# Kernel tuning notes

Measured on AMD Instinct MI355X. Metric: run time of the kernel, lower is better.

Reference implementation:

```python
import jax, jax.numpy as jnp
import numpy as np

N_NODES = 100000
N_EDGES = 1600000
IN_FEATS = 512
OUT_FEATS = 128


def setup_inputs() -> dict:
    key = jax.random.key(0)
    k1, k2, k3, k4, k5 = jax.random.split(key, 5)
    feat = jax.random.normal(k1, (N_NODES, IN_FEATS), dtype=jnp.float32)
    src = jax.random.randint(k2, (N_EDGES,), 0, N_NODES, dtype=jnp.int32)
    dst = jax.random.randint(k3, (N_EDGES,), 0, N_NODES, dtype=jnp.int32)
    edge_weight = jax.random.uniform(k4, (N_EDGES,), dtype=jnp.float32)
    # xavier_uniform init for the [in, out] weight
    limit = float(np.sqrt(6.0 / (IN_FEATS + OUT_FEATS)))
    weight = jax.random.uniform(k5, (IN_FEATS, OUT_FEATS), dtype=jnp.float32,
                                minval=-limit, maxval=limit)
    bias = jnp.zeros((OUT_FEATS,), dtype=jnp.float32)
    return {"feat": feat, "weight": weight, "bias": bias,
            "edge_weight": edge_weight, "src": src, "dst": dst}


def reference(feat, weight, bias, edge_weight, src, dst):
    n = feat.shape[0]
    ones = jnp.ones_like(edge_weight)
    # degrees from edge list; clamp(min=1)
    out_deg = jnp.maximum(jax.ops.segment_sum(ones, src, num_segments=n), 1.0)
    in_deg = jnp.maximum(jax.ops.segment_sum(ones, dst, num_segments=n), 1.0)
    # norm='both': left-normalize source feats by out_deg^-0.5
    feat_src = feat * jax.lax.rsqrt(out_deg)[:, None]
    # in_feats > out_feats -> project before aggregation
    h = feat_src @ weight                      # [N, OUT]
    msg = h[src] * edge_weight[:, None]        # u_mul_e, [E, OUT]
    rst = jax.ops.segment_sum(msg, dst, num_segments=n)  # fn.sum per dst
    # right-normalize by in_deg^-0.5, add bias (activation is None)
    rst = rst * jax.lax.rsqrt(in_deg)[:, None] + bias
    return rst
```

## Files before the change

### kernel.cpp

```cpp
#include <hip/hip_runtime.h>
#include <hip/hip_bf16.h>

#define NNODES 100000
#define NEDGES 1600000
#define INF 512
#define OUTF 128
#define NB 391
#define BCAP 5120
#define SEG 4096

typedef __attribute__((ext_vector_type(8))) __bf16 bf16x8;
typedef __attribute__((ext_vector_type(4))) float f32x4;
typedef __attribute__((ext_vector_type(2))) float f32x2;

__global__ void wt_kernel(const float* __restrict__ w, unsigned short* __restrict__ wt) {
  int i = blockIdx.x * blockDim.x + threadIdx.x;
  if (i < OUTF * INF) {
    int n = i >> 9;
    int k = i & 511;
    __bf16 b = (__bf16)(w[k * OUTF + n]);
    wt[i] = __builtin_bit_cast(unsigned short, b);
  }
}

__global__ __launch_bounds__(256) void bucket_kernel(
    const int* __restrict__ src, const int* __restrict__ dst,
    const float* __restrict__ ew, int* __restrict__ out_cnt,
    int* __restrict__ bucket_cnt, int2* __restrict__ bucket) {
  __shared__ int hist[NB];
  __shared__ int base[NB];
  int t = threadIdx.x;
  for (int i = t; i < NB; i += 256) hist[i] = 0;
  __syncthreads();
  int e0 = blockIdx.x * SEG;
  int e1 = min(e0 + SEG, NEDGES);
  for (int e = e0 + t; e < e1; e += 256) {
    atomicAdd(&out_cnt[src[e]], 1);
    atomicAdd(&hist[dst[e] >> 8], 1);
  }
  __syncthreads();
  for (int i = t; i < NB; i += 256) {
    int c = hist[i];
    base[i] = c ? atomicAdd(&bucket_cnt[i], c) : 0;
    hist[i] = 0;
  }
  __syncthreads();
  for (int e = e0 + t; e < e1; e += 256) {
    int d = dst[e];
    int b = d >> 8;
    int r = atomicAdd(&hist[b], 1);
    int2 en;
    en.x = ((d & 255) << 17) | src[e];
    en.y = __float_as_int(ew[e]);
    bucket[(size_t)b * BCAP + base[b] + r] = en;
  }
}

__global__ __launch_bounds__(512) void bscan_kernel(const int* __restrict__ bucket_cnt,
                                                    int* __restrict__ bucket_base,
                                                    int* __restrict__ rowptr) {
  __shared__ int s[512];
  int t = threadIdx.x;
  int v = (t < NB) ? bucket_cnt[t] : 0;
  s[t] = v;
  __syncthreads();
  for (int off = 1; off < 512; off <<= 1) {
    int x = (t >= off) ? s[t - off] : 0;
    __syncthreads();
    s[t] += x;
    __syncthreads();
  }
  if (t < NB) bucket_base[t] = s[t] - v;
  if (t == 0) rowptr[NNODES] = NEDGES;
}

__global__ __launch_bounds__(256) void csr_kernel(
    const int* __restrict__ bucket_cnt, const int* __restrict__ bucket_base,
    const int2* __restrict__ bucket, int* __restrict__ rowptr,
    int2* __restrict__ epair) {
  __shared__ int hist[256];
  __shared__ int cur[256];
  int b = blockIdx.x;
  int t = threadIdx.x;
  int nb = bucket_cnt[b];
  int bbase = bucket_base[b];
  const int2* bk = bucket + (size_t)b * BCAP;
  hist[t] = 0;
  __syncthreads();
  for (int i = t; i < nb; i += 256) atomicAdd(&hist[bk[i].x >> 17], 1);
  __syncthreads();
  int v = hist[t];
  for (int off = 1; off < 256; off <<= 1) {
    int x = (t >= off) ? hist[t - off] : 0;
    __syncthreads();
    hist[t] += x;
    __syncthreads();
  }
  int excl = hist[t] - v;
  int node = b * 256 + t;
  if (node < NNODES) rowptr[node] = bbase + excl;
  cur[t] = excl;
  __syncthreads();
  for (int i = t; i < nb; i += 256) {
    int2 en = bk[i];
    int nl = en.x >> 17;
    int r = atomicAdd(&cur[nl], 1);
    epair[bbase + r] = make_int2(en.x & 0x1FFFF, en.y);
  }
}

__global__ __launch_bounds__(256) void gemm_kernel(
    const float* __restrict__ feat, const unsigned short* __restrict__ wt,
    const int* __restrict__ out_cnt, unsigned short* __restrict__ h) {
  const int lane = threadIdx.x & 63;
  const int wave = threadIdx.x >> 6;
  const int l15 = lane & 15;
  const int lg  = lane >> 4;
  const int rowbase = blockIdx.x * 128 + wave * 32;

  int r0 = rowbase + l15;
  int r1 = rowbase + 16 + l15;
  float s0 = (r0 < NNODES) ? rsqrtf(fmaxf((float)out_cnt[r0], 1.0f)) : 0.0f;
  float s1 = (r1 < NNODES) ? rsqrtf(fmaxf((float)out_cnt[r1], 1.0f)) : 0.0f;
  const float* fp0 = feat + (size_t)(r0 < NNODES ? r0 : 0) * INF + lg * 8;
  const float* fp1 = feat + (size_t)(r1 < NNODES ? r1 : 0) * INF + lg * 8;

  f32x4 acc[2][8];
#pragma unroll
  for (int f = 0; f < 2; ++f)
#pragma unroll
    for (int c = 0; c < 8; ++c) acc[f][c] = (f32x4){0.f, 0.f, 0.f, 0.f};

#pragma unroll 2
  for (int k0 = 0; k0 < INF; k0 += 32) {
    f32x4 u0 = *(const f32x4*)(fp0 + k0);
    f32x4 v0 = *(const f32x4*)(fp0 + k0 + 4);
    f32x4 u1 = *(const f32x4*)(fp1 + k0);
    f32x4 v1 = *(const f32x4*)(fp1 + k0 + 4);
    bf16x8 a0, a1;
#pragma unroll
    for (int j = 0; j < 4; ++j) {
      a0[j]     = (__bf16)(u0[j] * s0);
      a0[j + 4] = (__bf16)(v0[j] * s0);
      a1[j]     = (__bf16)(u1[j] * s1);
      a1[j + 4] = (__bf16)(v1[j] * s1);
    }
    const unsigned short* bp = wt + l15 * INF + k0 + lg * 8;
#pragma unroll
    for (int c = 0; c < 8; ++c) {
      bf16x8 b = *(const bf16x8*)(bp + c * 16 * INF);
      acc[0][c] = __builtin_amdgcn_mfma_f32_16x16x32_bf16(a0, b, acc[0][c], 0, 0, 0);
      acc[1][c] = __builtin_amdgcn_mfma_f32_16x16x32_bf16(a1, b, acc[1][c], 0, 0, 0);
    }
  }

#pragma unroll
  for (int f = 0; f < 2; ++f) {
    int rb = rowbase + f * 16 + lg * 4;
#pragma unroll
    for (int r = 0; r < 4; ++r) {
      int row = rb + r;
      if (row < NNODES) {
#pragma unroll
        for (int c = 0; c < 8; ++c) {
          __bf16 bv = (__bf16)acc[f][c][r];
          h[(size_t)row * OUTF + c * 16 + l15] = __builtin_bit_cast(unsigned short, bv);
        }
      }
    }
  }
}

__global__ __launch_bounds__(256) void gather_kernel(
    const int* __restrict__ rowptr, const int2* __restrict__ epair,
    const unsigned short* __restrict__ h, const float* __restrict__ bias,
    float* __restrict__ out) {
  int node = (blockIdx.x * blockDim.x + threadIdx.x) >> 6;
  int lane = threadIdx.x & 63;
  if (node >= NNODES) return;
  int beg = rowptr[node];
  int end = rowptr[node + 1];

  float ax = 0.f, ay = 0.f;
  for (int base = beg; base < end; base += 64) {
    int j = base + lane;
    int2 pr = make_int2(0, 0);
    if (j < end) pr = epair[j];
    int cnt = min(end - base, 64);
    int t = 0;
    for (; t + 4 <= cnt; t += 4) {
      int s0 = __shfl(pr.x, t);
      int s1 = __shfl(pr.x, t + 1);
      int s2 = __shfl(pr.x, t + 2);
      int s3 = __shfl(pr.x, t + 3);
      float w0 = __int_as_float(__shfl(pr.y, t));
      float w1 = __int_as_float(__shfl(pr.y, t + 1));
      float w2 = __int_as_float(__shfl(pr.y, t + 2));
      float w3 = __int_as_float(__shfl(pr.y, t + 3));
      unsigned int u0 = *((const unsigned int*)(h + (size_t)s0 * OUTF) + lane);
      unsigned int u1 = *((const unsigned int*)(h + (size_t)s1 * OUTF) + lane);
      unsigned int u2 = *((const unsigned int*)(h + (size_t)s2 * OUTF) + lane);
      unsigned int u3 = *((const unsigned int*)(h + (size_t)s3 * OUTF) + lane);
      ax += __uint_as_float(u0 << 16) * w0 + __uint_as_float(u1 << 16) * w1 +
            __uint_as_float(u2 << 16) * w2 + __uint_as_float(u3 << 16) * w3;
      ay += __uint_as_float(u0 & 0xFFFF0000u) * w0 + __uint_as_float(u1 & 0xFFFF0000u) * w1 +
            __uint_as_float(u2 & 0xFFFF0000u) * w2 + __uint_as_float(u3 & 0xFFFF0000u) * w3;
    }
    for (; t < cnt; ++t) {
      int s = __shfl(pr.x, t);
      float w = __int_as_float(__shfl(pr.y, t));
      unsigned int u = *((const unsigned int*)(h + (size_t)s * OUTF) + lane);
      ax += __uint_as_float(u << 16) * w;
      ay += __uint_as_float(u & 0xFFFF0000u) * w;
    }
  }

  float sc = rsqrtf(fmaxf((float)(end - beg), 1.0f));
  f32x2 b = *((const f32x2*)bias + lane);
  f32x2 r;
  r.x = ax * sc + b.x;
  r.y = ay * sc + b.y;
  *((f32x2*)(out + (size_t)node * OUTF) + lane) = r;
}

extern "C" void kernel_launch(void* const* d_in, const int* in_sizes, int n_in,
                              void* d_out, int out_size, void* d_ws, size_t ws_size,
                              hipStream_t stream) {
  const float* feat   = (const float*)d_in[0];
  const float* weight = (const float*)d_in[1];
  const float* bias   = (const float*)d_in[2];
  const float* ew     = (const float*)d_in[3];
  const int*   src    = (const int*)d_in[4];
  const int*   dst    = (const int*)d_in[5];
  float* out = (float*)d_out;
  char* ws = (char*)d_ws;

  int* out_cnt        = (int*)ws;
  int* rowptr         = (int*)(ws + 0x80000);
  int* bucket_cnt     = (int*)(ws + 0x100000);
  int* bucket_base    = (int*)(ws + 0x101000);
  unsigned short* wt  = (unsigned short*)(ws + 0x110000);
  int2* bucket        = (int2*)(ws + 0x140000);
  int2* epair         = (int2*)(ws + 0x1200000);
  unsigned short* h   = (unsigned short*)(ws + 0x2000000);

  hipMemsetAsync(out_cnt, 0, NNODES * sizeof(int), stream);
  hipMemsetAsync(bucket_cnt, 0, NB * sizeof(int), stream);

  wt_kernel<<<(OUTF * INF + 255) / 256, 256, 0, stream>>>(weight, wt);
  bucket_kernel<<<(NEDGES + SEG - 1) / SEG, 256, 0, stream>>>(src, dst, ew, out_cnt,
                                                              bucket_cnt, bucket);
  bscan_kernel<<<1, 512, 0, stream>>>(bucket_cnt, bucket_base, rowptr);
  csr_kernel<<<NB, 256, 0, stream>>>(bucket_cnt, bucket_base, bucket, rowptr, epair);
  gemm_kernel<<<(NNODES + 127) / 128, 256, 0, stream>>>(feat, wt, out_cnt, h);
  gather_kernel<<<(NNODES * 64 + 255) / 256, 256, 0, stream>>>(rowptr, epair, h, bias, out);
}
```

Baseline: 284.8 us.

## Double-buffer GEMM tiles in LDS via direct global-to-LDS loads

The projection GEMM now stages feature rows and weight tiles into double-buffered shared memory using global_load_lds. The next K-slice is prefetched while MFMAs run on the current one, and an XOR swizzle on the A tile avoids bank conflicts. The weight pre-pass writes a fragment-ordered bf16 layout so each B tile is one contiguous copy. This targets the latency exposed by per-lane strided global loads, at the cost of an extra barrier per K step and 48KB of LDS per block, which limits occupancy.

Result: faster. 256.9 us (-9.8%).

```diff
diff --git a/kernel.cpp b/kernel.cpp
--- a/kernel.cpp
+++ b/kernel.cpp
@@ -8,19 +8,36 @@
 #define NB 391
 #define BCAP 5120
 #define SEG 4096
+#define BK 32
+#define NKSTEP (INF / BK)
 
 typedef __attribute__((ext_vector_type(8))) __bf16 bf16x8;
 typedef __attribute__((ext_vector_type(4))) float f32x4;
 typedef __attribute__((ext_vector_type(2))) float f32x2;
 
-__global__ void wt_kernel(const float* __restrict__ w, unsigned short* __restrict__ wt) {
+typedef const __attribute__((address_space(1))) unsigned int* gas_ptr;
+typedef __attribute__((address_space(3))) unsigned int* las_ptr;
+
+__device__ __forceinline__ void gload_lds16(const void* g, void* l) {
+  __builtin_amdgcn_global_load_lds((gas_ptr)g, (las_ptr)l, 16, 0, 0);
+}
+
+__global__ void wt_kernel(const float* __restrict__ w, unsigned short* __restrict__ wta) {
   int i = blockIdx.x * blockDim.x + threadIdx.x;
-  if (i < OUTF * INF) {
-    int n = i >> 9;
-    int k = i & 511;
-    __bf16 b = (__bf16)(w[k * OUTF + n]);
-    wt[i] = __builtin_bit_cast(unsigned short, b);
-  }
+  if (i >= 8192) return;
+  int lg  = i & 3;
+  int l15 = (i >> 2) & 15;
+  int c   = (i >> 6) & 7;
+  int kb  = i >> 9;
+  int n = c * 16 + l15;
+  int kbase = kb * 32 + lg * 8;
+  unsigned short tmp[8];
+#pragma unroll
+  for (int j = 0; j < 8; ++j) {
+    __bf16 b = (__bf16)(w[(size_t)(kbase + j) * OUTF + n]);
+    tmp[j] = __builtin_bit_cast(unsigned short, b);
+  }
+  ((int4*)wta)[i] = *(int4*)tmp;
 }
 
 __global__ __launch_bounds__(256) void bucket_kernel(
@@ -109,21 +126,26 @@
   }
 }
 
-__global__ __launch_bounds__(256) void gemm_kernel(
-    const float* __restrict__ feat, const unsigned short* __restrict__ wt,
+__global__ __launch_bounds__(256, 3) void gemm_kernel(
+    const float* __restrict__ feat, const unsigned short* __restrict__ wta,
     const int* __restrict__ out_cnt, unsigned short* __restrict__ h) {
-  const int lane = threadIdx.x & 63;
-  const int wave = threadIdx.x >> 6;
+  __shared__ float As[2][128 * BK];
+  __shared__ unsigned short Bs[2][4096];
+
+  const int t = threadIdx.x;
+  const int lane = t & 63;
+  const int wave = t >> 6;
   const int l15 = lane & 15;
   const int lg  = lane >> 4;
-  const int rowbase = blockIdx.x * 128 + wave * 32;
-
-  int r0 = rowbase + l15;
-  int r1 = rowbase + 16 + l15;
-  float s0 = (r0 < NNODES) ? rsqrtf(fmaxf((float)out_cnt[r0], 1.0f)) : 0.0f;
-  float s1 = (r1 < NNODES) ? rsqrtf(fmaxf((float)out_cnt[r1], 1.0f)) : 0.0f;
-  const float* fp0 = feat + (size_t)(r0 < NNODES ? r0 : 0) * INF + lg * 8;
-  const float* fp1 = feat + (size_t)(r1 < NNODES ? r1 : 0) * INF + lg * 8;
+  const int rowbase = blockIdx.x * 128;
+
+  const int srow_off = lane >> 3;
+  const int schunk = (lane & 7) ^ srow_off;
+
+  int r0 = rowbase + wave * 32 + l15;
+  int r1 = r0 + 16;
+  float s0 = rsqrtf(fmaxf((float)out_cnt[min(r0, NNODES - 1)], 1.0f));
+  float s1 = rsqrtf(fmaxf((float)out_cnt[min(r1, NNODES - 1)], 1.0f));
 
   f32x4 acc[2][8];
 #pragma unroll
@@ -131,32 +153,66 @@
 #pragma unroll
     for (int c = 0; c < 8; ++c) acc[f][c] = (f32x4){0.f, 0.f, 0.f, 0.f};
 
-#pragma unroll 2
-  for (int k0 = 0; k0 < INF; k0 += 32) {
-    f32x4 u0 = *(const f32x4*)(fp0 + k0);
-    f32x4 v0 = *(const f32x4*)(fp0 + k0 + 4);
-    f32x4 u1 = *(const f32x4*)(fp1 + k0);
-    f32x4 v1 = *(const f32x4*)(fp1 + k0 + 4);
-    bf16x8 a0, a1;
-#pragma unroll
-    for (int j = 0; j < 4; ++j) {
-      a0[j]     = (__bf16)(u0[j] * s0);
-      a0[j + 4] = (__bf16)(v0[j] * s0);
-      a1[j]     = (__bf16)(u1[j] * s1);
-      a1[j + 4] = (__bf16)(v1[j] * s1);
-    }
-    const unsigned short* bp = wt + l15 * INF + k0 + lg * 8;
+#define STAGE(buf, kb)                                                         \
+  {                                                                            \
+    _Pragma("unroll")                                                          \
+    for (int q = 0; q < 4; ++q) {                                              \
+      int gr = min(rowbase + wave * 32 + q * 8 + srow_off, NNODES - 1);        \
+      const float* gsrc = feat + (size_t)gr * INF + (kb) * BK + schunk * 4;    \
+      gload_lds16(gsrc, &As[buf][(wave * 4 + q) * 256]);                       \
+    }                                                                          \
+    _Pragma("unroll")                                                          \
+    for (int q = 0; q < 2; ++q) {                                              \
+      const unsigned short* gsrc =                                             \
+          wta + (size_t)(kb) * 4096 + (wave * 2 + q) * 512 + lane * 8;         \
+      gload_lds16(gsrc, &Bs[buf][(wave * 2 + q) * 512]);                       \
+    }                                                                          \
+  }
+
+  int buf = 0;
+  STAGE(0, 0);
+  __syncthreads();
+
+  for (int kb = 0; kb < NKSTEP; ++kb) {
+    if (kb + 1 < NKSTEP) STAGE(buf ^ 1, kb + 1);
+
+    bf16x8 bfr[8];
+#pragma unroll
+    for (int c = 0; c < 8; ++c)
+      bfr[c] = *(const bf16x8*)&Bs[buf][c * 512 + l15 * 32 + lg * 8];
+
+    bf16x8 afr[2];
+#pragma unroll
+    for (int rf = 0; rf < 2; ++rf) {
+      int r = wave * 32 + rf * 16 + l15;
+      int c0 = (lg * 2) ^ (l15 & 7);
+      int c1 = (lg * 2 + 1) ^ (l15 & 7);
+      f32x4 u = *(const f32x4*)&As[buf][r * 32 + c0 * 4];
+      f32x4 v = *(const f32x4*)&As[buf][r * 32 + c1 * 4];
+      float s = rf ? s1 : s0;
+      bf16x8 a;
+#pragma unroll
+      for (int j = 0; j < 4; ++j) {
+        a[j]     = (__bf16)(u[j] * s);
+        a[j + 4] = (__bf16)(v[j] * s);
+      }
+      afr[rf] = a;
+    }
+
 #pragma unroll
     for (int c = 0; c < 8; ++c) {
-      bf16x8 b = *(const bf16x8*)(bp + c * 16 * INF);
-      acc[0][c] = __builtin_amdgcn_mfma_f32_16x16x32_bf16(a0, b, acc[0][c], 0, 0, 0);
-      acc[1][c] = __builtin_amdgcn_mfma_f32_16x16x32_bf16(a1, b, acc[1][c], 0, 0, 0);
-    }
-  }
+      acc[0][c] = __builtin_amdgcn_mfma_f32_16x16x32_bf16(afr[0], bfr[c], acc[0][c], 0, 0, 0);
+      acc[1][c] = __builtin_amdgcn_mfma_f32_16x16x32_bf16(afr[1], bfr[c], acc[1][c], 0, 0, 0);
+    }
+
+    __syncthreads();
+    buf ^= 1;
+  }
+#undef STAGE
 
 #pragma unroll
   for (int f = 0; f < 2; ++f) {
-    int rb = rowbase + f * 16 + lg * 4;
+    int rb = rowbase + wave * 32 + f * 16 + lg * 4;
 #pragma unroll
     for (int r = 0; r < 4; ++r) {
       int row = rb + r;
@@ -239,7 +295,7 @@
   int* rowptr         = (int*)(ws + 0x80000);
   int* bucket_cnt     = (int*)(ws + 0x100000);
   int* bucket_base    = (int*)(ws + 0x101000);
-  unsigned short* wt  = (unsigned short*)(ws + 0x110000);
+  unsigned short* wta = (unsigned short*)(ws + 0x110000);
   int2* bucket        = (int2*)(ws + 0x140000);
   int2* epair         = (int2*)(ws + 0x1200000);
   unsigned short* h   = (unsigned short*)(ws + 0x2000000);
@@ -247,11 +303,11 @@
   hipMemsetAsync(out_cnt, 0, NNODES * sizeof(int), stream);
   hipMemsetAsync(bucket_cnt, 0, NB * sizeof(int), stream);
 
-  wt_kernel<<<(OUTF * INF + 255) / 256, 256, 0, stream>>>(weight, wt);
+  wt_kernel<<<32, 256, 0, stream>>>(weight, wta);
   bucket_kernel<<<(NEDGES + SEG - 1) / SEG, 256, 0, stream>>>(src, dst, ew, out_cnt,
                                                               bucket_cnt, bucket);
   bscan_kernel<<<1, 512, 0, stream>>>(bucket_cnt, bucket_base, rowptr);
   csr_kernel<<<NB, 256, 0, stream>>>(bucket_cnt, bucket_base, bucket, rowptr, epair);
-  gemm_kernel<<<(NNODES + 127) / 128, 256, 0, stream>>>(feat, wt, out_cnt, h);
+  gemm_kernel<<<(NNODES + 127) / 128, 256, 0, stream>>>(feat, wta, out_cnt, h);
   gather_kernel<<<(NNODES * 64 + 255) / 256, 256, 0, stream>>>(rowptr, epair, h, bias, out);
 }
```
